# Performance work log

Hardware: AMD Instinct MI355X
Metric: run time of the kernel (lower is better)

Reference implementation:

```python
import jax, jax.numpy as jnp
import numpy as np


def conv1x1(x, w, b):
    # x: [B,Cin,H,W], w: [Cout,Cin], b: [Cout]
    return jnp.einsum('bchw,oc->bohw', x, w) + b[None, :, None, None]


def _lin_idx_w(in_size, out_size):
    # PyTorch bilinear, align_corners=False: src = max((i+0.5)*scale - 0.5, 0)
    scale = in_size / out_size
    src = jnp.maximum((jnp.arange(out_size, dtype=jnp.float32) + 0.5) * scale - 0.5, 0.0)
    i0 = jnp.floor(src).astype(jnp.int32)
    i0 = jnp.minimum(i0, in_size - 1)
    i1 = jnp.minimum(i0 + 1, in_size - 1)
    w1 = src - i0.astype(jnp.float32)
    return i0, i1, w1


def bilinear_resize(x, out_h, out_w):
    Hin, Win = x.shape[-2], x.shape[-1]
    y0, y1, wy = _lin_idx_w(Hin, out_h)
    x0, x1, wx = _lin_idx_w(Win, out_w)
    wy = wy[:, None]  # [out_h,1]
    rows = x[:, :, y0, :] * (1.0 - wy) + x[:, :, y1, :] * wy
    out = rows[:, :, :, x0] * (1.0 - wx) + rows[:, :, :, x1] * wx      # [B,C,out_h,out_w]
    return out


def setup_inputs() -> dict:
    key = jax.random.key(0)
    ks = jax.random.split(key, 10)
    C, C8 = 512, 64
    s = 1.0 / np.sqrt(C)
    return {
        'content': jax.random.normal(ks[0], (4, C, 64, 64), jnp.float32),
        'style': jax.random.normal(ks[1], (4, C, 80, 80), jnp.float32),
        'f_w': jax.random.normal(ks[2], (C8, C), jnp.float32) * s,
        'f_b': jax.random.normal(ks[3], (C8,), jnp.float32) * 0.01,
        'g_w': jax.random.normal(ks[4], (C8, C), jnp.float32) * s,
        'g_b': jax.random.normal(ks[5], (C8,), jnp.float32) * 0.01,
        'h_w': jax.random.normal(ks[6], (C, C), jnp.float32) * s,
        'h_b': jax.random.normal(ks[7], (C,), jnp.float32) * 0.01,
        'out_w': jax.random.normal(ks[8], (C, C), jnp.float32) * s,
        'out_b': jax.random.normal(ks[9], (C,), jnp.float32) * 0.01,
    }


def reference(content, style, f_w, f_b, g_w, g_b, h_w, h_b, out_w, out_b):
    B, C, H, W = content.shape
    HW = H * W
    f = conv1x1(content, f_w, f_b).reshape(B, -1, HW)                       # [B,C8,HW] (query, pre-transpose)
    g = bilinear_resize(conv1x1(style, g_w, g_b), H, W).reshape(B, -1, HW)  # [B,C8,HW]
    h = bilinear_resize(conv1x1(style, h_w, h_b), H, W).reshape(B, C, HW)   # [B,C,HW]
    attn = jax.nn.softmax(jnp.einsum('bcm,bcn->bmn', f, g), axis=-1)        # [B,HW_q,HW_k]
    out = jnp.einsum('bcn,bmn->bcm', h, attn).reshape(B, C, H, W)
    return conv1x1(out, out_w, out_b)
```

## Files before the change

kernel.cpp:

```cpp
#include <hip/hip_runtime.h>

#define NB 4
#define NC 512
#define ND 64
#define HW 4096
#define SPIN 6400

typedef _Float16 f16;
typedef _Float16 f16x8 __attribute__((ext_vector_type(8)));
typedef short s16x8 __attribute__((ext_vector_type(8)));
typedef short s16x4 __attribute__((ext_vector_type(4)));
typedef float f32x4 __attribute__((ext_vector_type(4)));
typedef float f32x16 __attribute__((ext_vector_type(16)));
typedef unsigned short ushortT;

__device__ __forceinline__ unsigned short f32_to_bf16(float x) {
  union { float f; unsigned u; } v; v.f = x;
  unsigned r = v.u + 0x7FFFu + ((v.u >> 16) & 1u);
  return (unsigned short)(r >> 16);
}

__device__ __forceinline__ void stv(float* p, float v) { *p = v; }
__device__ __forceinline__ void stv(f16* p, float v) { *p = (f16)v; }
__device__ __forceinline__ void stv(unsigned short* p, float v) { *p = f32_to_bf16(v); }

__device__ __forceinline__ unsigned cvt_pk_bf16(float lo, float hi) {
  unsigned r;
  asm("v_cvt_pk_bf16_f32 %0, %1, %2" : "=v"(r) : "v"(lo), "v"(hi));
  return r;
}

__global__ __launch_bounds__(256) void cvtw_kernel(const float* __restrict__ fw,
                                                   const float* __restrict__ gw,
                                                   const float* __restrict__ hw,
                                                   const float* __restrict__ ow,
                                                   f16* __restrict__ dst) {
  int i = blockIdx.x * 256 + threadIdx.x;
  const float* src; int off;
  if (i < 32768) { src = fw; off = 0; }
  else if (i < 65536) { src = gw; off = 32768; }
  else if (i < 327680) { src = hw; off = 65536; }
  else { src = ow; off = 327680; }
  dst[i] = (f16)src[i - off];
}

__global__ __launch_bounds__(256) void tcvt_kernel(const float* __restrict__ in,
                                                   f16* __restrict__ out) {
  __shared__ float Xs[64][65];
  int p0 = blockIdx.x * 64, c0 = blockIdx.y * 64, b = blockIdx.z;
  int t = threadIdx.x;
  const float* ib = in + ((size_t)b * NC + c0) * HW + p0;
  int pl = t & 63, cg = t >> 6;
#pragma unroll
  for (int k = 0; k < 16; ++k) {
    int c = cg * 16 + k;
    Xs[c][pl] = ib[(size_t)c * HW + pl];
  }
  __syncthreads();
  int p = t >> 2, cb = (t & 3) * 16;
  union { f16 h[16]; float4 q[2]; } u;
#pragma unroll
  for (int j = 0; j < 16; ++j) u.h[j] = (f16)Xs[cb + j][p];
  f16* ob = out + ((size_t)b * HW + p0 + p) * NC + c0 + cb;
  *(float4*)(ob) = u.q[0];
  *(float4*)(ob + 8) = u.q[1];
}

__global__ __launch_bounds__(256) void rstcvt_kernel(const float* __restrict__ X,
                                                     f16* __restrict__ Y) {
  __shared__ float Xs[64 * 165];
  int oy = blockIdx.x, c0 = blockIdx.y * 64, b = blockIdx.z;
  float syf = fmaxf((oy + 0.5f) * 1.25f - 0.5f, 0.f);
  int y0 = (int)syf; int y1 = min(y0 + 1, 79); float wy = syf - (float)y0;
  int t = threadIdx.x;
  const float* Xb = X + ((size_t)b * NC + c0) * SPIN;
#pragma unroll
  for (int k = 0; k < 10; ++k) {
    int idx = t + k * 256;
    int c = idx / 40;
    int rem = idx - c * 40;
    int yy = rem / 20;
    int x4 = rem - yy * 20;
    int ysrc = yy ? y1 : y0;
    float4 v = *(const float4*)(Xb + (size_t)c * SPIN + ysrc * 80 + x4 * 4);
    float* d = Xs + c * 165 + yy * 82 + x4 * 4;
    d[0] = v.x; d[1] = v.y; d[2] = v.z; d[3] = v.w;
  }
  __syncthreads();
  int ox = t >> 2, cb = (t & 3) * 16;
  float sxf = fmaxf((ox + 0.5f) * 1.25f - 0.5f, 0.f);
  int x0 = (int)sxf; int x1 = min(x0 + 1, 79); float wx = sxf - (float)x0;
  union { f16 h[16]; float4 q[2]; } u;
#pragma unroll
  for (int j = 0; j < 16; ++j) {
    const float* base = Xs + (cb + j) * 165;
    float a0 = base[x0], a1 = base[x1];
    float b0 = base[82 + x0], b1 = base[82 + x1];
    float r0 = a0 + (a1 - a0) * wx;
    float r1 = b0 + (b1 - b0) * wx;
    u.h[j] = (f16)(r0 + (r1 - r0) * wy);
  }
  f16* ob = Y + ((size_t)b * HW + oy * 64 + ox) * NC + c0 + cb;
  *(float4*)(ob) = u.q[0];
  *(float4*)(ob + 8) = u.q[1];
}

__global__ __launch_bounds__(256) void convpm2_kernel(const f16* __restrict__ X0,
                                                      const f16* __restrict__ X1,
                                                      const f16* __restrict__ W01,
                                                      const float* __restrict__ b0,
                                                      const float* __restrict__ b1,
                                                      f16* __restrict__ Y0,
                                                      f16* __restrict__ Y1) {
  int sel = blockIdx.z >> 2;
  int b = blockIdx.z & 3;
  const f16* X = sel ? X1 : X0;
  const f16* W = W01 + sel * (ND * NC);
  const float* bias = sel ? b1 : b0;
  f16* Y = sel ? Y1 : Y0;
  int t = threadIdx.x, l = t & 63, w = t >> 6;
  int pw = blockIdx.x * 256 + w * 64;
  int l4 = l & 15, g = l >> 4;
  f32x4 acc[4][4] = {};
  const f16* Xb = X + ((size_t)b * HW + pw) * NC;
  for (int kk = 0; kk < 16; ++kk) {
    int co = kk * 32 + g * 8;
    f16x8 a[4], bb[4];
#pragma unroll
    for (int ms = 0; ms < 4; ++ms) a[ms] = *(const f16x8*)(Xb + (size_t)(ms * 16 + l4) * NC + co);
#pragma unroll
    for (int ct = 0; ct < 4; ++ct) bb[ct] = *(const f16x8*)(W + (size_t)(ct * 16 + l4) * NC + co);
#pragma unroll
    for (int ms = 0; ms < 4; ++ms)
#pragma unroll
      for (int ct = 0; ct < 4; ++ct)
        acc[ms][ct] = __builtin_amdgcn_mfma_f32_16x16x32_f16(a[ms], bb[ct], acc[ms][ct], 0, 0, 0);
  }
  float bv[4];
#pragma unroll
  for (int ct = 0; ct < 4; ++ct) bv[ct] = bias[ct * 16 + l4];
  f16* Yb = Y + ((size_t)b * HW + pw) * ND;
#pragma unroll
  for (int ms = 0; ms < 4; ++ms)
#pragma unroll
    for (int ct = 0; ct < 4; ++ct)
#pragma unroll
      for (int r = 0; r < 4; ++r)
        Yb[(size_t)(ms * 16 + g * 4 + r) * ND + ct * 16 + l4] = (f16)(acc[ms][ct][r] + bv[ct]);
}

template <typename OUT_T>
__global__ __launch_bounds__(256) void convcm_kernel(const f16* __restrict__ X,
                                                     const f16* __restrict__ W,
                                                     const float* __restrict__ bias,
                                                     OUT_T* __restrict__ Y, int O) {
  int b = blockIdx.z;
  int o0 = blockIdx.x * 64;
  int t = threadIdx.x, l = t & 63, w = t >> 6;
  int pw = blockIdx.y * 256 + w * 64;
  int l4 = l & 15, g = l >> 4;
  f32x4 acc[4][4] = {};
  const f16* Xb = X + ((size_t)b * HW + pw) * NC;
  const f16* Wb = W + (size_t)o0 * NC;
  for (int kk = 0; kk < 16; ++kk) {
    int co = kk * 32 + g * 8;
    f16x8 a[4], bb[4];
#pragma unroll
    for (int ms = 0; ms < 4; ++ms) a[ms] = *(const f16x8*)(Wb + (size_t)(ms * 16 + l4) * NC + co);
#pragma unroll
    for (int ct = 0; ct < 4; ++ct) bb[ct] = *(const f16x8*)(Xb + (size_t)(ct * 16 + l4) * NC + co);
#pragma unroll
    for (int ms = 0; ms < 4; ++ms)
#pragma unroll
      for (int ct = 0; ct < 4; ++ct)
        acc[ms][ct] = __builtin_amdgcn_mfma_f32_16x16x32_f16(a[ms], bb[ct], acc[ms][ct], 0, 0, 0);
  }
  float bv[4][4];
#pragma unroll
  for (int ms = 0; ms < 4; ++ms)
#pragma unroll
    for (int r = 0; r < 4; ++r) bv[ms][r] = bias[o0 + ms * 16 + g * 4 + r];
#pragma unroll
  for (int ms = 0; ms < 4; ++ms)
#pragma unroll
    for (int ct = 0; ct < 4; ++ct)
#pragma unroll
      for (int r = 0; r < 4; ++r) {
        float val = acc[ms][ct][r] + bv[ms][r];
        stv(&Y[((size_t)b * O + o0 + ms * 16 + g * 4 + r) * HW + pw + ct * 16 + l4], val);
      }
}

union PAu { unsigned u[4]; s16x8 v; };
union VSu { s16x8 v; s16x4 h[2]; };

__global__ __launch_bounds__(256, 3) void attn_kernel(const f16* __restrict__ FT,
                                                      const f16* __restrict__ GT,
                                                      const unsigned short* __restrict__ HC,
                                                      f16* __restrict__ MIDT) {
  __shared__ __align__(16) char Vs[2][16384];
  int bid = blockIdx.x;
  int b = (bid & 7) >> 1;
  int cs = bid & 1;
  int mt = bid >> 3;
  int t = threadIdx.x, l = t & 63, w = t >> 6;
  int lm = l & 31, hf = l >> 5;
  int mf = w >> 1, cq = w & 1;
  int mr = mt * 64 + mf * 32;
  int cqb = cq * 128;

  const f16* Fq = FT + ((size_t)b * HW + mr + lm) * ND + hf * 8;
  f16x8 q[4];
#pragma unroll
  for (int kc = 0; kc < 4; ++kc) q[kc] = *(const f16x8*)(Fq + kc * 16);

  const f16* kp = GT + (size_t)b * HW * ND + (size_t)lm * ND + hf * 8;

  int c0 = t >> 2;
  int seg = t & 3;
  int kn_s = seg >> 1, half = seg & 1;
  int swz = c0 & 3;
  const int offA = (((kn_s * 2) ^ swz) << 4) + half * 8;
  const int offB = (((kn_s * 2 + 1) ^ swz) << 4) + half * 8;
  const int wbase = c0 * 64;
  const unsigned short* vsrc = HC + ((size_t)b * NC + cs * 256 + c0) * HW + seg * 8;

  const int rb = (cqb + lm) * 64;
  const int ro0 = (((0 * 2 + hf) ^ (lm & 3)) << 4);
  const int ro1 = (((1 * 2 + hf) ^ (lm & 3)) << 4);

  f32x16 acc[4] = {};
  float den = 0.f;

#define STAGE_LOAD(n0x)                                                      \
  do {                                                                       \
    _Pragma("unroll") for (int r_ = 0; r_ < 4; ++r_)                         \
        vreg[r_].v = *(const s16x8*)(vsrc + (size_t)r_ * 64 * HW + (n0x));   \
  } while (0)

#define STAGE_WRITE(bufidx)                                                  \
  do {                                                                       \
    char* base_ = Vs[bufidx] + wbase;                                        \
    _Pragma("unroll") for (int r_ = 0; r_ < 4; ++r_) {                       \
      *(s16x4*)(base_ + r_ * 4096 + offA) = vreg[r_].h[0];                   \
      *(s16x4*)(base_ + r_ * 4096 + offB) = vreg[r_].h[1];                   \
    }                                                                        \
  } while (0)

  {
    VSu vreg[4];
    STAGE_LOAD(0);
    STAGE_WRITE(0);
  }
  __syncthreads();

  for (int it = 0; it < 128; ++it) {
    const int n0 = it * 32;
    f16x8 kb[4];
#pragma unroll
    for (int kc = 0; kc < 4; ++kc)
      kb[kc] = *(const f16x8*)(kp + (size_t)n0 * ND + kc * 16);
    VSu vreg[4];
    if (it < 127) STAGE_LOAD(n0 + 32);
    f32x16 s = {};
#pragma unroll
    for (int kc = 0; kc < 4; ++kc)
      s = __builtin_amdgcn_mfma_f32_32x32x16_f16(kb[kc], q[kc], s, 0, 0, 0);
    float p[16];
#pragma unroll
    for (int r = 0; r < 16; ++r) { p[r] = __expf(s[r]); den += p[r]; }
    PAu pa[2];
    pa[0].u[0] = cvt_pk_bf16(p[0], p[1]);
    pa[0].u[1] = cvt_pk_bf16(p[2], p[3]);
    pa[0].u[2] = cvt_pk_bf16(p[4], p[5]);
    pa[0].u[3] = cvt_pk_bf16(p[6], p[7]);
    pa[1].u[0] = cvt_pk_bf16(p[8], p[9]);
    pa[1].u[1] = cvt_pk_bf16(p[10], p[11]);
    pa[1].u[2] = cvt_pk_bf16(p[12], p[13]);
    pa[1].u[3] = cvt_pk_bf16(p[14], p[15]);
    const char* Vc = Vs[it & 1];
#pragma unroll
    for (int cf = 0; cf < 4; ++cf) {
      const char* vr = Vc + rb + cf * 2048;
      s16x8 v0 = *(const s16x8*)(vr + ro0);
      s16x8 v1 = *(const s16x8*)(vr + ro1);
      __builtin_amdgcn_s_setprio(1);
      acc[cf] = __builtin_amdgcn_mfma_f32_32x32x16_bf16(pa[0].v, v0, acc[cf], 0, 0, 0);
      acc[cf] = __builtin_amdgcn_mfma_f32_32x32x16_bf16(pa[1].v, v1, acc[cf], 0, 0, 0);
      __builtin_amdgcn_s_setprio(0);
    }
    if (it < 127) STAGE_WRITE((it + 1) & 1);
    __syncthreads();
  }
#undef STAGE_LOAD
#undef STAGE_WRITE

  den += __shfl_xor(den, 32);
  float rd = 1.f / den;
  f16* Mb = MIDT + ((size_t)b * HW + mr) * NC + cs * 256 + cqb + lm;
#pragma unroll
  for (int r = 0; r < 16; ++r) {
    int mrow = (r & 3) + 8 * (r >> 2) + 4 * hf;
    float rv = __shfl(rd, mrow);
#pragma unroll
    for (int cf = 0; cf < 4; ++cf)
      Mb[(size_t)mrow * NC + cf * 32] = (f16)(acc[cf][r] * rv);
  }
}

extern "C" void kernel_launch(void* const* d_in, const int* in_sizes, int n_in,
                              void* d_out, int out_size, void* d_ws, size_t ws_size,
                              hipStream_t stream) {
  const float* content = (const float*)d_in[0];
  const float* style   = (const float*)d_in[1];
  const float* f_w = (const float*)d_in[2];
  const float* f_b = (const float*)d_in[3];
  const float* g_w = (const float*)d_in[4];
  const float* g_b = (const float*)d_in[5];
  const float* h_w = (const float*)d_in[6];
  const float* h_b = (const float*)d_in[7];
  const float* out_w = (const float*)d_in[8];
  const float* out_b = (const float*)d_in[9];
  float* out = (float*)d_out;

  const size_t MB = 1ull << 20;
  char* base = (char*)d_ws;
  f16* contentT = (f16*)base;
  f16* midT     = (f16*)base;
  unsigned short* hC = (unsigned short*)(base + 16 * MB);
  f16* fT = (f16*)(base + 32 * MB);
  f16* gT = (f16*)(base + 34 * MB);
  f16* styrT = (f16*)(base + 48 * MB);
  f16* w16 = (f16*)(base + 64 * MB);
  f16* fw16 = w16;
  f16* gw16 = w16 + 32768;
  f16* hw16 = w16 + 65536;
  f16* ow16 = w16 + 327680;

  cvtw_kernel<<<dim3(589824 / 256), 256, 0, stream>>>(f_w, g_w, h_w, out_w, w16);
  tcvt_kernel<<<dim3(HW / 64, NC / 64, NB), 256, 0, stream>>>(content, contentT);
  rstcvt_kernel<<<dim3(64, NC / 64, NB), 256, 0, stream>>>(style, styrT);
  convpm2_kernel<<<dim3(HW / 256, 1, 2 * NB), 256, 0, stream>>>(contentT, styrT, fw16, f_b, g_b, fT, gT);
  convcm_kernel<unsigned short><<<dim3(NC / 64, HW / 256, NB), 256, 0, stream>>>(styrT, hw16, h_b, hC, NC);
  attn_kernel<<<dim3(512), 256, 0, stream>>>(fT, gT, hC, midT);
  convcm_kernel<float><<<dim3(NC / 64, HW / 256, NB), 256, 0, stream>>>(midT, ow16, out_b, out, NC);
}
```

Before: 299.4 us.

## Retile attention kernel to 128-channel blocks with 64-key steps and padded LDS

Each attention block now covers 128 output channels instead of 256, so the grid doubles to 1024 blocks and launch bounds rise to 4 blocks per CU. Each iteration processes 64 keys (two QK^T MFMA tiles) before the PV MFMAs. This halves the number of barriers and uses a padded, row-contiguous LDS layout (144-byte stride) in place of the XOR swizzle. The cost is that QK^T and exp are recomputed across twice as many channel blocks, and the per-thread load pattern changes to contiguous 64-byte row segments.

Result: slower. 411.8 us (+37.6%).

```diff
diff --git a/kernel.cpp b/kernel.cpp
--- a/kernel.cpp
+++ b/kernel.cpp
@@ -194,20 +194,22 @@
 union PAu { unsigned u[4]; s16x8 v; };
 union VSu { s16x8 v; s16x4 h[2]; };
 
-__global__ __launch_bounds__(256, 3) void attn_kernel(const f16* __restrict__ FT,
+__global__ __launch_bounds__(256, 4) void attn_kernel(const f16* __restrict__ FT,
                                                       const f16* __restrict__ GT,
                                                       const unsigned short* __restrict__ HC,
                                                       f16* __restrict__ MIDT) {
-  __shared__ __align__(16) char Vs[2][16384];
+  __shared__ __align__(16) char Vs[2][18432];
   int bid = blockIdx.x;
   int b = (bid & 7) >> 1;
-  int cs = bid & 1;
-  int mt = bid >> 3;
+  int lowb = bid & 1;
+  int idx = bid >> 3;
+  int mt = idx & 63;
+  int cblk = ((idx >> 6) << 1) | lowb;
   int t = threadIdx.x, l = t & 63, w = t >> 6;
   int lm = l & 31, hf = l >> 5;
   int mf = w >> 1, cq = w & 1;
   int mr = mt * 64 + mf * 32;
-  int cqb = cq * 128;
+  int cbase = cblk * 128;
 
   const f16* Fq = FT + ((size_t)b * HW + mr + lm) * ND + hf * 8;
   f16x8 q[4];
@@ -216,35 +218,46 @@
 
   const f16* kp = GT + (size_t)b * HW * ND + (size_t)lm * ND + hf * 8;
 
-  int c0 = t >> 2;
-  int seg = t & 3;
-  int kn_s = seg >> 1, half = seg & 1;
-  int swz = c0 & 3;
-  const int offA = (((kn_s * 2) ^ swz) << 4) + half * 8;
-  const int offB = (((kn_s * 2 + 1) ^ swz) << 4) + half * 8;
-  const int wbase = c0 * 64;
-  const unsigned short* vsrc = HC + ((size_t)b * NC + cs * 256 + c0) * HW + seg * 8;
-
-  const int rb = (cqb + lm) * 64;
-  const int ro0 = (((0 * 2 + hf) ^ (lm & 3)) << 4);
-  const int ro1 = (((1 * 2 + hf) ^ (lm & 3)) << 4);
-
-  f32x16 acc[4] = {};
+  int cr = t >> 1, hn = t & 1;
+  const unsigned short* vsrc = HC + ((size_t)b * NC + cbase + cr) * HW + hn * 32;
+  const int wb = cr * 144 + hn * 64;
+
+  const int rbase = (cq * 64 + lm) * 144 + hf * 16;
+
+  f32x16 acc[2] = {};
   float den = 0.f;
 
 #define STAGE_LOAD(n0x)                                                      \
   do {                                                                       \
-    _Pragma("unroll") for (int r_ = 0; r_ < 4; ++r_)                         \
-        vreg[r_].v = *(const s16x8*)(vsrc + (size_t)r_ * 64 * HW + (n0x));   \
+    _Pragma("unroll") for (int i_ = 0; i_ < 4; ++i_)                         \
+        vreg[i_].v = *(const s16x8*)(vsrc + (n0x) + i_ * 8);                 \
   } while (0)
 
 #define STAGE_WRITE(bufidx)                                                  \
   do {                                                                       \
-    char* base_ = Vs[bufidx] + wbase;                                        \
-    _Pragma("unroll") for (int r_ = 0; r_ < 4; ++r_) {                       \
-      *(s16x4*)(base_ + r_ * 4096 + offA) = vreg[r_].h[0];                   \
-      *(s16x4*)(base_ + r_ * 4096 + offB) = vreg[r_].h[1];                   \
+    char* B_ = Vs[bufidx] + wb;                                              \
+    _Pragma("unroll") for (int i_ = 0; i_ < 4; ++i_) {                       \
+      int o_ = (i_ >> 1) * 32 + (i_ & 1) * 8;                                \
+      *(s16x4*)(B_ + o_) = vreg[i_].h[0];                                    \
+      *(s16x4*)(B_ + o_ + 16) = vreg[i_].h[1];                               \
     }                                                                        \
+  } while (0)
+
+#define PACK(sv, o)                                                          \
+  do {                                                                       \
+    float p_[16];                                                            \
+    _Pragma("unroll") for (int r_ = 0; r_ < 16; ++r_) {                      \
+      p_[r_] = __expf(sv[r_]);                                               \
+      den += p_[r_];                                                         \
+    }                                                                        \
+    pa[o].u[0] = cvt_pk_bf16(p_[0], p_[1]);                                  \
+    pa[o].u[1] = cvt_pk_bf16(p_[2], p_[3]);                                  \
+    pa[o].u[2] = cvt_pk_bf16(p_[4], p_[5]);                                  \
+    pa[o].u[3] = cvt_pk_bf16(p_[6], p_[7]);                                  \
+    pa[o + 1].u[0] = cvt_pk_bf16(p_[8], p_[9]);                              \
+    pa[o + 1].u[1] = cvt_pk_bf16(p_[10], p_[11]);                            \
+    pa[o + 1].u[2] = cvt_pk_bf16(p_[12], p_[13]);                            \
+    pa[o + 1].u[3] = cvt_pk_bf16(p_[14], p_[15]);                            \
   } while (0)
 
   {
@@ -254,56 +267,64 @@
   }
   __syncthreads();
 
-  for (int it = 0; it < 128; ++it) {
-    const int n0 = it * 32;
-    f16x8 kb[4];
-#pragma unroll
-    for (int kc = 0; kc < 4; ++kc)
-      kb[kc] = *(const f16x8*)(kp + (size_t)n0 * ND + kc * 16);
+  for (int it = 0; it < 64; ++it) {
+    const int n0 = it * 64;
+    PAu pa[4];
+    {
+      f16x8 kb[4];
+#pragma unroll
+      for (int kc = 0; kc < 4; ++kc)
+        kb[kc] = *(const f16x8*)(kp + (size_t)n0 * ND + kc * 16);
+      f32x16 s = {};
+#pragma unroll
+      for (int kc = 0; kc < 4; ++kc)
+        s = __builtin_amdgcn_mfma_f32_32x32x16_f16(kb[kc], q[kc], s, 0, 0, 0);
+      PACK(s, 0);
+    }
+    {
+      f16x8 kb[4];
+#pragma unroll
+      for (int kc = 0; kc < 4; ++kc)
+        kb[kc] = *(const f16x8*)(kp + (size_t)(n0 + 32) * ND + kc * 16);
+      f32x16 s = {};
+#pragma unroll
+      for (int kc = 0; kc < 4; ++kc)
+        s = __builtin_amdgcn_mfma_f32_32x32x16_f16(kb[kc], q[kc], s, 0, 0, 0);
+      PACK(s, 2);
+    }
     VSu vreg[4];
-    if (it < 127) STAGE_LOAD(n0 + 32);
-    f32x16 s = {};
-#pragma unroll
-    for (int kc = 0; kc < 4; ++kc)
-      s = __builtin_amdgcn_mfma_f32_32x32x16_f16(kb[kc], q[kc], s, 0, 0, 0);
-    float p[16];
-#pragma unroll
-    for (int r = 0; r < 16; ++r) { p[r] = __expf(s[r]); den += p[r]; }
-    PAu pa[2];
-    pa[0].u[0] = cvt_pk_bf16(p[0], p[1]);
-    pa[0].u[1] = cvt_pk_bf16(p[2], p[3]);
-    pa[0].u[2] = cvt_pk_bf16(p[4], p[5]);
-    pa[0].u[3] = cvt_pk_bf16(p[6], p[7]);
-    pa[1].u[0] = cvt_pk_bf16(p[8], p[9]);
-    pa[1].u[1] = cvt_pk_bf16(p[10], p[11]);
-    pa[1].u[2] = cvt_pk_bf16(p[12], p[13]);
-    pa[1].u[3] = cvt_pk_bf16(p[14], p[15]);
+    if (it < 63) STAGE_LOAD(n0 + 64);
     const char* Vc = Vs[it & 1];
 #pragma unroll
-    for (int cf = 0; cf < 4; ++cf) {
-      const char* vr = Vc + rb + cf * 2048;
-      s16x8 v0 = *(const s16x8*)(vr + ro0);
-      s16x8 v1 = *(const s16x8*)(vr + ro1);
+    for (int cf = 0; cf < 2; ++cf) {
+      const char* vr = Vc + rbase + cf * 4608;
+      s16x8 v0 = *(const s16x8*)(vr);
+      s16x8 v1 = *(const s16x8*)(vr + 32);
+      s16x8 v2 = *(const s16x8*)(vr + 64);
+      s16x8 v3 = *(const s16x8*)(vr + 96);
       __builtin_amdgcn_s_setprio(1);
       acc[cf] = __builtin_amdgcn_mfma_f32_32x32x16_bf16(pa[0].v, v0, acc[cf], 0, 0, 0);
       acc[cf] = __builtin_amdgcn_mfma_f32_32x32x16_bf16(pa[1].v, v1, acc[cf], 0, 0, 0);
+      acc[cf] = __builtin_amdgcn_mfma_f32_32x32x16_bf16(pa[2].v, v2, acc[cf], 0, 0, 0);
+      acc[cf] = __builtin_amdgcn_mfma_f32_32x32x16_bf16(pa[3].v, v3, acc[cf], 0, 0, 0);
       __builtin_amdgcn_s_setprio(0);
     }
-    if (it < 127) STAGE_WRITE((it + 1) & 1);
+    if (it < 63) STAGE_WRITE((it + 1) & 1);
     __syncthreads();
   }
 #undef STAGE_LOAD
 #undef STAGE_WRITE
+#undef PACK
 
   den += __shfl_xor(den, 32);
   float rd = 1.f / den;
-  f16* Mb = MIDT + ((size_t)b * HW + mr) * NC + cs * 256 + cqb + lm;
+  f16* Mb = MIDT + ((size_t)b * HW + mr) * NC + cbase + cq * 64 + lm;
 #pragma unroll
   for (int r = 0; r < 16; ++r) {
     int mrow = (r & 3) + 8 * (r >> 2) + 4 * hf;
     float rv = __shfl(rd, mrow);
 #pragma unroll
-    for (int cf = 0; cf < 4; ++cf)
+    for (int cf = 0; cf < 2; ++cf)
       Mb[(size_t)mrow * NC + cf * 32] = (f16)(acc[cf][r] * rv);
   }
 }
@@ -342,6 +363,6 @@
   rstcvt_kernel<<<dim3(64, NC / 64, NB), 256, 0, stream>>>(style, styrT);
   convpm2_kernel<<<dim3(HW / 256, 1, 2 * NB), 256, 0, stream>>>(contentT, styrT, fw16, f_b, g_b, fT, gT);
   convcm_kernel<unsigned short><<<dim3(NC / 64, HW / 256, NB), 256, 0, stream>>>(styrT, hw16, h_b, hC, NC);
-  attn_kernel<<<dim3(512), 256, 0, stream>>>(fT, gT, hC, midT);
+  attn_kernel<<<dim3(1024), 256, 0, stream>>>(fT, gT, hC, midT);
   convcm_kernel<float><<<dim3(NC / 64, HW / 256, NB), 256, 0, stream>>>(midT, ow16, out_b, out, NC);
 }
```

## Software-pipeline attention loop with 64-key tiles, exp2 softmax, wider swizzled LDS

Applied to the files above, without the earlier changes.

Restructures the attention main loop to process 64 keys per iteration with two QK MFMA tiles, and software-pipelines it so the PV MFMAs of the previous tile overlap the QK and exp of the current tile. Queries are prescaled by log2(e) so exp2 can be used, and K fragments are register double-buffered. The V staging buffer doubles to 64KB with a new XOR swizzle, and occupancy drops from 3 to 2 blocks per CU. This aims to hide exp/latency stalls and halve barrier count, at the cost of more registers and LDS and fewer resident waves. Prescaling q in fp16 adds a small rounding change.

Measured after the change: 285.5 us. 4.6% less time.

```diff
diff --git a/kernel.cpp b/kernel.cpp
--- a/kernel.cpp
+++ b/kernel.cpp
@@ -29,6 +29,12 @@
   asm("v_cvt_pk_bf16_f32 %0, %1, %2" : "=v"(r) : "v"(lo), "v"(hi));
   return r;
 }
+
+#if __has_builtin(__builtin_amdgcn_exp2f)
+#define EXP2F(x) __builtin_amdgcn_exp2f(x)
+#else
+#define EXP2F(x) exp2f(x)
+#endif
 
 __global__ __launch_bounds__(256) void cvtw_kernel(const float* __restrict__ fw,
                                                    const float* __restrict__ gw,
@@ -194,11 +200,11 @@
 union PAu { unsigned u[4]; s16x8 v; };
 union VSu { s16x8 v; s16x4 h[2]; };
 
-__global__ __launch_bounds__(256, 3) void attn_kernel(const f16* __restrict__ FT,
+__global__ __launch_bounds__(256, 2) void attn_kernel(const f16* __restrict__ FT,
                                                       const f16* __restrict__ GT,
                                                       const unsigned short* __restrict__ HC,
                                                       f16* __restrict__ MIDT) {
-  __shared__ __align__(16) char Vs[2][16384];
+  __shared__ __align__(16) char Vs[2][32768];
   int bid = blockIdx.x;
   int b = (bid & 7) >> 1;
   int cs = bid & 1;
@@ -211,89 +217,147 @@
 
   const f16* Fq = FT + ((size_t)b * HW + mr + lm) * ND + hf * 8;
   f16x8 q[4];
-#pragma unroll
-  for (int kc = 0; kc < 4; ++kc) q[kc] = *(const f16x8*)(Fq + kc * 16);
-
-  const f16* kp = GT + (size_t)b * HW * ND + (size_t)lm * ND + hf * 8;
-
-  int c0 = t >> 2;
-  int seg = t & 3;
-  int kn_s = seg >> 1, half = seg & 1;
-  int swz = c0 & 3;
-  const int offA = (((kn_s * 2) ^ swz) << 4) + half * 8;
-  const int offB = (((kn_s * 2 + 1) ^ swz) << 4) + half * 8;
-  const int wbase = c0 * 64;
-  const unsigned short* vsrc = HC + ((size_t)b * NC + cs * 256 + c0) * HW + seg * 8;
-
-  const int rb = (cqb + lm) * 64;
-  const int ro0 = (((0 * 2 + hf) ^ (lm & 3)) << 4);
-  const int ro1 = (((1 * 2 + hf) ^ (lm & 3)) << 4);
+  {
+    const f16 l2e = (f16)1.44269504f;
+#pragma unroll
+    for (int kc = 0; kc < 4; ++kc) {
+      f16x8 v = *(const f16x8*)(Fq + kc * 16);
+#pragma unroll
+      for (int j = 0; j < 8; ++j) v[j] *= l2e;
+      q[kc] = v;
+    }
+  }
+
+  const f16* kp0 = GT + (size_t)b * HW * ND + (size_t)lm * ND + hf * 8;
+  const f16* kp1 = kp0 + 32 * ND;
+
+  int scv = t >> 2;
+  int nsg = (t & 3) * 16;
+  const unsigned short* vp0 = HC + ((size_t)b * NC + cs * 256 + scv) * HW + nsg;
+  const unsigned short* vp1 = vp0 + (size_t)64 * HW;
+  const unsigned short* vp2 = vp0 + (size_t)128 * HW;
+  const unsigned short* vp3 = vp0 + (size_t)192 * HW;
+
+  int sb0 = (t & 3) * 32;
+  int swv = (scv & 7) << 4;
+  char* wa = Vs[0] + scv * 128 + (sb0 ^ swv);
+  char* wb = Vs[0] + scv * 128 + ((sb0 + 16) ^ swv);
+
+  int cl0 = cqb + lm;
+  int vsw = (lm & 7) << 4;
+  const char* r0 = Vs[0] + cl0 * 128 + ((0 + hf * 16) ^ vsw);
+  const char* r1 = Vs[0] + cl0 * 128 + ((32 + hf * 16) ^ vsw);
+  const char* r2 = Vs[0] + cl0 * 128 + ((64 + hf * 16) ^ vsw);
+  const char* r3 = Vs[0] + cl0 * 128 + ((96 + hf * 16) ^ vsw);
 
   f32x16 acc[4] = {};
   float den = 0.f;
 
-#define STAGE_LOAD(n0x)                                                      \
-  do {                                                                       \
-    _Pragma("unroll") for (int r_ = 0; r_ < 4; ++r_)                         \
-        vreg[r_].v = *(const s16x8*)(vsrc + (size_t)r_ * 64 * HW + (n0x));   \
-  } while (0)
-
-#define STAGE_WRITE(bufidx)                                                  \
-  do {                                                                       \
-    char* base_ = Vs[bufidx] + wbase;                                        \
-    _Pragma("unroll") for (int r_ = 0; r_ < 4; ++r_) {                       \
-      *(s16x4*)(base_ + r_ * 4096 + offA) = vreg[r_].h[0];                   \
-      *(s16x4*)(base_ + r_ * 4096 + offB) = vreg[r_].h[1];                   \
-    }                                                                        \
+#define KLOAD(KN)                                                          \
+  do {                                                                     \
+    _Pragma("unroll") for (int kc = 0; kc < 4; ++kc) {                     \
+      KN[0][kc] = *(const f16x8*)(kp0 + kc * 16);                          \
+      KN[1][kc] = *(const f16x8*)(kp1 + kc * 16);                          \
+    }                                                                      \
+    kp0 += 64 * ND; kp1 += 64 * ND;                                        \
+  } while (0)
+
+#define VLOAD()                                                            \
+  do {                                                                     \
+    vreg[0].v = *(const s16x8*)(vp0); vreg[1].v = *(const s16x8*)(vp0 + 8);\
+    vreg[2].v = *(const s16x8*)(vp1); vreg[3].v = *(const s16x8*)(vp1 + 8);\
+    vreg[4].v = *(const s16x8*)(vp2); vreg[5].v = *(const s16x8*)(vp2 + 8);\
+    vreg[6].v = *(const s16x8*)(vp3); vreg[7].v = *(const s16x8*)(vp3 + 8);\
+    vp0 += 64; vp1 += 64; vp2 += 64; vp3 += 64;                            \
+  } while (0)
+
+#define VWRITE(BOFF)                                                       \
+  do {                                                                     \
+    _Pragma("unroll") for (int r_ = 0; r_ < 4; ++r_) {                     \
+      *(s16x4*)(wa + (BOFF) + r_ * 8192) = vreg[2 * r_].h[0];              \
+      *(s16x4*)(wb + (BOFF) + r_ * 8192) = vreg[2 * r_].h[1];              \
+      *(s16x4*)(wa + (BOFF) + r_ * 8192 + 8) = vreg[2 * r_ + 1].h[0];      \
+      *(s16x4*)(wb + (BOFF) + r_ * 8192 + 8) = vreg[2 * r_ + 1].h[1];      \
+    }                                                                      \
+  } while (0)
+
+#define PACK(sv, PA, o)                                                    \
+  do {                                                                     \
+    float p_[16];                                                          \
+    _Pragma("unroll") for (int r_ = 0; r_ < 16; ++r_) p_[r_] = EXP2F(sv[r_]); \
+    float d0_ = (p_[0] + p_[1]) + (p_[2] + p_[3]);                         \
+    float d1_ = (p_[4] + p_[5]) + (p_[6] + p_[7]);                         \
+    float d2_ = (p_[8] + p_[9]) + (p_[10] + p_[11]);                       \
+    float d3_ = (p_[12] + p_[13]) + (p_[14] + p_[15]);                     \
+    den += (d0_ + d1_) + (d2_ + d3_);                                      \
+    PA[o].u[0] = cvt_pk_bf16(p_[0], p_[1]);                                \
+    PA[o].u[1] = cvt_pk_bf16(p_[2], p_[3]);                                \
+    PA[o].u[2] = cvt_pk_bf16(p_[4], p_[5]);                                \
+    PA[o].u[3] = cvt_pk_bf16(p_[6], p_[7]);                                \
+    PA[o + 1].u[0] = cvt_pk_bf16(p_[8], p_[9]);                            \
+    PA[o + 1].u[1] = cvt_pk_bf16(p_[10], p_[11]);                          \
+    PA[o + 1].u[2] = cvt_pk_bf16(p_[12], p_[13]);                          \
+    PA[o + 1].u[3] = cvt_pk_bf16(p_[14], p_[15]);                          \
+  } while (0)
+
+#define PVBODY(PA, BOFF)                                                   \
+  do {                                                                     \
+    _Pragma("unroll") for (int cf = 0; cf < 4; ++cf) {                     \
+      s16x8 v0_ = *(const s16x8*)(r0 + (BOFF) + cf * 4096);                \
+      s16x8 v1_ = *(const s16x8*)(r1 + (BOFF) + cf * 4096);                \
+      s16x8 v2_ = *(const s16x8*)(r2 + (BOFF) + cf * 4096);                \
+      s16x8 v3_ = *(const s16x8*)(r3 + (BOFF) + cf * 4096);                \
+      __builtin_amdgcn_s_setprio(1);                                       \
+      acc[cf] = __builtin_amdgcn_mfma_f32_32x32x16_bf16(PA[0].v, v0_, acc[cf], 0, 0, 0); \
+      acc[cf] = __builtin_amdgcn_mfma_f32_32x32x16_bf16(PA[1].v, v1_, acc[cf], 0, 0, 0); \
+      acc[cf] = __builtin_amdgcn_mfma_f32_32x32x16_bf16(PA[2].v, v2_, acc[cf], 0, 0, 0); \
+      acc[cf] = __builtin_amdgcn_mfma_f32_32x32x16_bf16(PA[3].v, v3_, acc[cf], 0, 0, 0); \
+      __builtin_amdgcn_s_setprio(0);                                       \
+    }                                                                      \
+  } while (0)
+
+#define ITER(PC, PP, KC, KN, BOFF, PRE, DOPV)                              \
+  do {                                                                     \
+    VSu vreg[8];                                                           \
+    if (PRE) { KLOAD(KN); VLOAD(); }                                       \
+    f32x16 s0 = {}, s1 = {};                                               \
+    __builtin_amdgcn_s_setprio(1);                                         \
+    _Pragma("unroll") for (int kc = 0; kc < 4; ++kc)                       \
+        s0 = __builtin_amdgcn_mfma_f32_32x32x16_f16(KC[0][kc], q[kc], s0, 0, 0, 0); \
+    _Pragma("unroll") for (int kc = 0; kc < 4; ++kc)                       \
+        s1 = __builtin_amdgcn_mfma_f32_32x32x16_f16(KC[1][kc], q[kc], s1, 0, 0, 0); \
+    __builtin_amdgcn_s_setprio(0);                                         \
+    if (DOPV) PVBODY(PP, BOFF);                                            \
+    PACK(s0, PC, 0);                                                       \
+    PACK(s1, PC, 2);                                                       \
+    __syncthreads();                                                       \
+    if (PRE) VWRITE(BOFF);                                                 \
   } while (0)
 
   {
-    VSu vreg[4];
-    STAGE_LOAD(0);
-    STAGE_WRITE(0);
-  }
+    VSu vreg[8];
+    VLOAD();
+    VWRITE(0);
+  }
+  f16x8 kbA[2][4], kbB[2][4];
+  KLOAD(kbA);
   __syncthreads();
 
-  for (int it = 0; it < 128; ++it) {
-    const int n0 = it * 32;
-    f16x8 kb[4];
-#pragma unroll
-    for (int kc = 0; kc < 4; ++kc)
-      kb[kc] = *(const f16x8*)(kp + (size_t)n0 * ND + kc * 16);
-    VSu vreg[4];
-    if (it < 127) STAGE_LOAD(n0 + 32);
-    f32x16 s = {};
-#pragma unroll
-    for (int kc = 0; kc < 4; ++kc)
-      s = __builtin_amdgcn_mfma_f32_32x32x16_f16(kb[kc], q[kc], s, 0, 0, 0);
-    float p[16];
-#pragma unroll
-    for (int r = 0; r < 16; ++r) { p[r] = __expf(s[r]); den += p[r]; }
-    PAu pa[2];
-    pa[0].u[0] = cvt_pk_bf16(p[0], p[1]);
-    pa[0].u[1] = cvt_pk_bf16(p[2], p[3]);
-    pa[0].u[2] = cvt_pk_bf16(p[4], p[5]);
-    pa[0].u[3] = cvt_pk_bf16(p[6], p[7]);
-    pa[1].u[0] = cvt_pk_bf16(p[8], p[9]);
-    pa[1].u[1] = cvt_pk_bf16(p[10], p[11]);
-    pa[1].u[2] = cvt_pk_bf16(p[12], p[13]);
-    pa[1].u[3] = cvt_pk_bf16(p[14], p[15]);
-    const char* Vc = Vs[it & 1];
-#pragma unroll
-    for (int cf = 0; cf < 4; ++cf) {
-      const char* vr = Vc + rb + cf * 2048;
-      s16x8 v0 = *(const s16x8*)(vr + ro0);
-      s16x8 v1 = *(const s16x8*)(vr + ro1);
-      __builtin_amdgcn_s_setprio(1);
-      acc[cf] = __builtin_amdgcn_mfma_f32_32x32x16_bf16(pa[0].v, v0, acc[cf], 0, 0, 0);
-      acc[cf] = __builtin_amdgcn_mfma_f32_32x32x16_bf16(pa[1].v, v1, acc[cf], 0, 0, 0);
-      __builtin_amdgcn_s_setprio(0);
-    }
-    if (it < 127) STAGE_WRITE((it + 1) & 1);
-    __syncthreads();
-  }
-#undef STAGE_LOAD
-#undef STAGE_WRITE
+  PAu paA[4], paB[4];
+  ITER(paA, paB, kbA, kbB, 32768, true, false);
+  for (int ito = 0; ito < 31; ++ito) {
+    ITER(paB, paA, kbB, kbA, 0, true, true);
+    ITER(paA, paB, kbA, kbB, 32768, true, true);
+  }
+  ITER(paB, paA, kbB, kbA, 0, false, true);
+  PVBODY(paB, 32768);
+
+#undef KLOAD
+#undef VLOAD
+#undef VWRITE
+#undef PACK
+#undef PVBODY
+#undef ITER
 
   den += __shfl_xor(den, 32);
   float rd = 1.f / den;
```
